# Optimization experiments

Measured on AMD Instinct MI355X. Metric: run time of the kernel, lower is better.

## Reference

```python
import jax, jax.numpy as jnp
import numpy as np

# model dims
B, S, R, D = 2, 64, 2048, 1024      # batch, num_bars(summary len), reg seq len, embed dim
H, KVH, HD = 16, 4, 64              # q heads, kv heads, head dim
G = H // KVH                        # GQA group size
KVD = KVH * HD
TPB = R // S                        # tokens per bar = 32
SCALE = HD ** -0.5
NEG = -1e9


def _rotate_half(x):
    x1, x2 = jnp.split(x, 2, axis=-1)
    return jnp.concatenate([-x2, x1], axis=-1)


def _apply_rope(q, k, cos, sin):
    return q * cos + _rotate_half(q) * sin, k * cos + _rotate_half(k) * sin


def _rope_1d(seq_len):
    # standard RoPE tables, shape (1, 1, seq_len, HD)
    inv = 1.0 / (10000.0 ** (jnp.arange(0, HD, 2, dtype=jnp.float32) / HD))
    freqs = jnp.arange(seq_len, dtype=jnp.float32)[:, None] * inv
    emb = jnp.concatenate([freqs, freqs], axis=-1)
    return jnp.cos(emb)[None, None], jnp.sin(emb)[None, None]


def _rope_2d(bar_ids, tib):
    # hierarchical 2D RoPE: half the rotary freqs encode bar id, half encode token-in-bar id
    q4 = HD // 4
    inv = 1.0 / (10000.0 ** (jnp.arange(q4, dtype=jnp.float32) * 2.0 / (HD // 2)))
    fb = bar_ids.astype(jnp.float32)[..., None] * inv   # (B, R, HD/4)
    ft = tib.astype(jnp.float32)[..., None] * inv       # (B, R, HD/4)
    freqs = jnp.concatenate([fb, ft], axis=-1)          # (B, R, HD/2)
    emb = jnp.concatenate([freqs, freqs], axis=-1)      # (B, R, HD)
    return jnp.cos(emb)[:, None], jnp.sin(emb)[:, None]


def _attn(q, k, v, mask):
    # masked softmax attention; mask (Lq, Lk) broadcast over batch/heads
    s = jnp.einsum('bhqd,bhkd->bhqk', q, k) * SCALE
    s = jnp.where(mask[None, None], s, NEG)
    p = jax.nn.softmax(s, axis=-1)
    return jnp.einsum('bhqk,bhkd->bhqd', p, v)


def _lin(x, w, b):
    return x @ w + b


def _heads(x, n):
    b, l, _ = x.shape
    return x.reshape(b, l, n, HD).transpose(0, 2, 1, 3)


def _merge(x):
    b, h, l, _ = x.shape
    return x.transpose(0, 2, 1, 3).reshape(b, l, h * HD)


PARAM_SHAPES = [('w_sq', (D, D)), ('b_sq', (D,)), ('w_sk', (D, KVD)), ('b_sk', (KVD,)),
                ('w_sv', (D, KVD)), ('b_sv', (KVD,)), ('w_so', (D, D)), ('b_so', (D,)),
                ('w_rq', (D, D)), ('b_rq', (D,)), ('w_rk', (D, KVD)), ('b_rk', (KVD,)),
                ('w_rv', (D, KVD)), ('b_rv', (KVD,)), ('w_ro', (D, D)), ('b_ro', (D,)),
                ('w_k2', (D, KVD)), ('b_k2', (KVD,)), ('w_v2', (D, KVD)), ('b_v2', (KVD,))]


def setup_inputs() -> dict:
    key = jax.random.key(0)
    ks = jax.random.split(key, 2 + len(PARAM_SHAPES))
    inp = {}
    inp['sum_x'] = jax.random.normal(ks[0], (B, S, D), jnp.float32)
    inp['reg_x'] = jax.random.normal(ks[1], (B, R, D), jnp.float32)
    for i, (n, shp) in enumerate(PARAM_SHAPES):
        inp[n] = jax.random.normal(ks[2 + i], shp, jnp.float32) * 0.02
    pos = jnp.arange(R)
    bar = pos // TPB
    tib = pos % TPB
    inp['bar_ids'] = jnp.tile(bar[None], (B, 1)).astype(jnp.int32)
    inp['token_in_bar_ids'] = jnp.tile(tib[None], (B, 1)).astype(jnp.int32)
    # summarize phase: summary-bar i attends to summary j<=i and regular tokens in bars<=i
    key_bar = jnp.concatenate([jnp.arange(S), bar])
    inp['summarize_block_mask'] = key_bar[None, :] <= jnp.arange(S)[:, None]
    # updating phase: regular token t attends to summary-K2 of bars<=bar(t) and regular s<=t
    upd = jnp.concatenate([jnp.arange(S)[None, :] <= bar[:, None],
                           pos[None, :] <= pos[:, None]], axis=1)
    inp['updating_block_mask'] = upd
    return inp


def reference(sum_x, reg_x, w_sq, b_sq, w_sk, b_sk, w_sv, b_sv, w_so, b_so,
              w_rq, b_rq, w_rk, b_rk, w_rv, b_rv, w_ro, b_ro, w_k2, b_k2, w_v2, b_v2,
              summarize_block_mask, updating_block_mask, bar_ids, token_in_bar_ids):
    sum_q = _heads(_lin(sum_x, w_sq, b_sq), H)
    sum_k = _heads(_lin(sum_x, w_sk, b_sk), KVH)
    sum_v = _heads(_lin(sum_x, w_sv, b_sv), KVH)
    reg_q = _heads(_lin(reg_x, w_rq, b_rq), H)
    reg_k = _heads(_lin(reg_x, w_rk, b_rk), KVH)
    reg_v = _heads(_lin(reg_x, w_rv, b_rv), KVH)
    # 1D RoPE for summary tokens, 2D hierarchical RoPE for regular tokens
    cos, sin = _rope_1d(S)
    sum_q, sum_k = _apply_rope(sum_q, sum_k, cos, sin)
    rcos, rsin = _rope_2d(bar_ids, token_in_bar_ids)
    reg_q, reg_k = _apply_rope(reg_q, reg_k, rcos, rsin)
    rep = lambda t: jnp.repeat(t, G, axis=1)  # GQA repeat_interleave over heads
    reg_k_r, reg_v_r = rep(reg_k), rep(reg_v)
    # phase 1: summarize (summary queries over [summary; regular] keys)
    cat_k = jnp.concatenate([rep(sum_k), reg_k_r], axis=2)
    cat_v = jnp.concatenate([rep(sum_v), reg_v_r], axis=2)
    sum_attn = _merge(_attn(sum_q, cat_k, cat_v, summarize_block_mask))  # (B, S, D)
    # phase 2: updating (regular queries over [summary K2/V2; regular] keys)
    k2 = rep(_heads(_lin(sum_attn, w_k2, b_k2), KVH))
    v2 = rep(_heads(_lin(sum_attn, w_v2, b_v2), KVH))
    cat_k2 = jnp.concatenate([k2, reg_k_r], axis=2)
    cat_v2 = jnp.concatenate([v2, reg_v_r], axis=2)
    reg_attn = _merge(_attn(reg_q, cat_k2, cat_v2, updating_block_mask))  # (B, R, D)
    return _lin(sum_attn, w_so, b_so), _lin(reg_attn, w_ro, b_ro)
```

## Files before the change

### kernel.cpp

```cpp
#include <hip/hip_runtime.h>

typedef unsigned short u16;
typedef __attribute__((ext_vector_type(8))) short s8v;
typedef __attribute__((ext_vector_type(4))) float f4v;

#define B_    2
#define S_    64
#define R_    2048
#define D_    1024
#define H_    16
#define KVH_  4
#define LOG2_10K 13.287712379549449f
#define QSC_  0.18033688011112042f

__device__ __forceinline__ u16 f2bf(float f) {
  union { float f; unsigned int i; } v; v.f = f;
  unsigned int x = v.i;
  return (u16)((x + 0x7FFFu + ((x >> 16) & 1u)) >> 16);
}
__device__ __forceinline__ u16 f2bf_ru(float f) {
  union { float f; unsigned int i; } v; v.f = f;
  return (u16)((v.i + 0x8000u) >> 16);
}

__device__ __forceinline__ f4v mfma2(const s8v& a0, const s8v& a1,
                                     const s8v& b0, const s8v& b1) {
  f4v t = {0.f, 0.f, 0.f, 0.f};
  t = __builtin_amdgcn_mfma_f32_16x16x32_bf16(a0, b0, t, 0, 0, 0);
  t = __builtin_amdgcn_mfma_f32_16x16x32_bf16(a1, b1, t, 0, 0, 0);
  return t;
}

struct WT10 { const float* w[10]; u16* o[10]; int C[10]; };

__global__ __launch_bounds__(256)
void transw_k(WT10 ws, const float* __restrict__ xa, const float* __restrict__ xb,
              u16* __restrict__ oa, u16* __restrict__ ob)
{
  const int z = blockIdx.z;
  if (z == 10) {
    int gid = blockIdx.x + blockIdx.y * 32;
    #pragma unroll
    for (int it = 0; it < 3; it++) {
      int idx = gid * 256 + threadIdx.x + it * 262144;
      if (idx < 540672) {
        int i = idx * 8;
        const float* src; u16* dst; int off;
        if (i < 131072) { src = xa; dst = oa; off = i; }
        else            { src = xb; dst = ob; off = i - 131072; }
        float4 a = *(const float4*)(src + off);
        float4 b = *(const float4*)(src + off + 4);
        s8v r;
        r[0] = (short)f2bf(a.x); r[1] = (short)f2bf(a.y);
        r[2] = (short)f2bf(a.z); r[3] = (short)f2bf(a.w);
        r[4] = (short)f2bf(b.x); r[5] = (short)f2bf(b.y);
        r[6] = (short)f2bf(b.z); r[7] = (short)f2bf(b.w);
        *(s8v*)(dst + off) = r;
      }
    }
    return;
  }
  const int C = ws.C[z];
  const int c0 = blockIdx.x * 32, k0 = blockIdx.y * 32;
  if (c0 >= C) return;
  __shared__ float t[32][33];
  const float* w = ws.w[z];
  u16* o = ws.o[z];
  const int x = threadIdx.x & 31, y = threadIdx.x >> 5;
  #pragma unroll
  for (int j = 0; j < 4; j++)
    t[y + 8 * j][x] = w[(size_t)(k0 + y + 8 * j) * C + c0 + x];
  __syncthreads();
  #pragma unroll
  for (int j = 0; j < 4; j++)
    o[(size_t)(c0 + y + 8 * j) * 1024 + k0 + x] = f2bf(t[x][y + 8 * j]);
}

__device__ __forceinline__ void gemm_core_db(
    const u16* __restrict__ Xrow, const u16* __restrict__ WTrow,
    u16 (*Adb)[72], u16 (*Bdb)[72], f4v (&acc)[2][4],
    int tid, int l15, int l4, int wro, int wco)
{
  s8v pa[2], pb[2];
  #pragma unroll
  for (int it = 0; it < 2; it++) {
    int seg = tid + it * 512;
    int r = seg >> 3, sg = (seg & 7) * 8;
    pa[it] = *(const s8v*)(Xrow  + (size_t)r * 1024 + sg);
    pb[it] = *(const s8v*)(WTrow + (size_t)r * 1024 + sg);
  }
  #pragma unroll
  for (int it = 0; it < 2; it++) {
    int seg = tid + it * 512;
    int r = seg >> 3, sg = (seg & 7) * 8;
    *(s8v*)&Adb[r][sg] = pa[it];
    *(s8v*)&Bdb[r][sg] = pb[it];
  }
  __syncthreads();

  #pragma unroll 2
  for (int k = 0; k < 16; k++) {
    const int off = (k & 1) * 128;
    if (k + 1 < 16) {
      const int k0 = (k + 1) * 64;
      #pragma unroll
      for (int it = 0; it < 2; it++) {
        int seg = tid + it * 512;
        int r = seg >> 3, sg = (seg & 7) * 8;
        pa[it] = *(const s8v*)(Xrow  + (size_t)r * 1024 + k0 + sg);
        pb[it] = *(const s8v*)(WTrow + (size_t)r * 1024 + k0 + sg);
      }
    }
    s8v af[2][2], bf4[4][2];
    #pragma unroll
    for (int rc = 0; rc < 2; rc++) {
      af[rc][0] = *(const s8v*)&Adb[off + wro + rc * 16 + l15][l4 * 8];
      af[rc][1] = *(const s8v*)&Adb[off + wro + rc * 16 + l15][32 + l4 * 8];
    }
    #pragma unroll
    for (int cc = 0; cc < 4; cc++) {
      bf4[cc][0] = *(const s8v*)&Bdb[off + wco + cc * 16 + l15][l4 * 8];
      bf4[cc][1] = *(const s8v*)&Bdb[off + wco + cc * 16 + l15][32 + l4 * 8];
    }
    #pragma unroll
    for (int rc = 0; rc < 2; rc++)
      #pragma unroll
      for (int cc = 0; cc < 4; cc++) {
        acc[rc][cc] = __builtin_amdgcn_mfma_f32_16x16x32_bf16(af[rc][0], bf4[cc][0], acc[rc][cc], 0, 0, 0);
        acc[rc][cc] = __builtin_amdgcn_mfma_f32_16x16x32_bf16(af[rc][1], bf4[cc][1], acc[rc][cc], 0, 0, 0);
      }
    if (k + 1 < 16) {
      const int noff = ((k + 1) & 1) * 128;
      #pragma unroll
      for (int it = 0; it < 2; it++) {
        int seg = tid + it * 512;
        int r = seg >> 3, sg = (seg & 7) * 8;
        *(s8v*)&Adb[noff + r][sg] = pa[it];
        *(s8v*)&Bdb[noff + r][sg] = pb[it];
      }
    }
    __syncthreads();
  }
}

__device__ __forceinline__ void epi_to_lds(
    const f4v (&acc)[2][4], const float* __restrict__ Bp, u16* __restrict__ Es,
    int cbr, int wro, int wco, int grb, int LB,
    int ropeMode, bool rope2d, bool sc, int l15, int l4)
{
  float bv[4];
  #pragma unroll
  for (int cc = 0; cc < 4; cc++) bv[cc] = Bp[cbr + cc * 16 + l15];

  if (ropeMode == 0) {
    #pragma unroll
    for (int rc = 0; rc < 2; rc++)
      #pragma unroll
      for (int reg = 0; reg < 4; reg++) {
        int lrow = wro + rc * 16 + l4 * 4 + reg;
        #pragma unroll
        for (int cc = 0; cc < 4; cc++)
          Es[lrow * 136 + wco + cc * 16 + l15] = f2bf(acc[rc][cc][reg] + bv[cc]);
      }
  } else {
    float step = rope2d ? (LOG2_10K / 16.f) : (LOG2_10K / 32.f);
    float inv_lo = exp2f(-(float)l15 * step);
    float inv_hi = rope2d ? inv_lo : inv_lo * exp2f(-16.f * step);
    #pragma unroll
    for (int rc = 0; rc < 2; rc++)
      #pragma unroll
      for (int reg = 0; reg < 4; reg++) {
        int lrow = wro + rc * 16 + l4 * 4 + reg;
        int grow = grb + lrow;
        int pos = grow & (LB - 1);
        int bar = pos >> 5, tib = pos & 31;
        #pragma unroll
        for (int cc = 0; cc < 4; cc++) {
          float inv = (cc & 1) ? inv_hi : inv_lo;
          float bse = rope2d ? (float)((cc & 1) ? tib : bar) : (float)pos;
          float ang = bse * inv;
          float sn, cs;
          sincosf(ang, &sn, &cs);
          float v0 = acc[rc][cc][reg] + bv[cc];
          float v1 = acc[rc][cc ^ 2][reg] + bv[cc ^ 2];
          float rot = (cc < 2) ? -v1 : v1;
          float val = v0 * cs + rot * sn;
          if (sc) val *= QSC_;
          Es[lrow * 136 + wco + cc * 16 + l15] = f2bf(val);
        }
      }
  }
}

__device__ __forceinline__ void store_tile_bf16(
    const u16* __restrict__ Es, u16* __restrict__ out,
    int grb, int c0r, int NH, int LB, int LBS, int tid)
{
  #pragma unroll
  for (int it = 0; it < 4; it++) {
    int idx = it * 512 + tid;
    int r = idx >> 4, ch = idx & 15;
    int grow = grb + r;
    int b = grow >> LBS, pos = grow & (LB - 1);
    int cg = c0r + ch * 8;
    size_t base = (((size_t)b * NH + (cg >> 6)) * LB + pos) * 64 + (cg & 63);
    *(s8v*)(out + base) = *(const s8v*)(Es + r * 136 + ch * 8);
  }
}

__device__ __forceinline__ void store_tile_vT(
    const u16* __restrict__ Es, u16* __restrict__ outT,
    int grb, int kvbase, int LB, int LBS, int tid)
{
  #pragma unroll
  for (int it = 0; it < 4; it++) {
    int idx = tid + it * 512;
    int dcol = idx & 127, rg = idx >> 7;
    int grow = grb + rg * 8;
    int b = grow >> LBS, pos = grow & (LB - 1);
    u16 tmp[8];
    #pragma unroll
    for (int j = 0; j < 8; j++) tmp[j] = Es[(rg * 8 + j) * 136 + dcol];
    u16* dst = outT + (((size_t)(b * KVH_ + kvbase + (dcol >> 6))) * 64 + (dcol & 63)) * LB + pos;
    *(s8v*)dst = *(s8v*)tmp;
  }
}

struct QkvA {
  const u16 *X, *WTs, *WTr;
  const float *b0s, *b1s, *b2s, *b0r, *b1r, *b2r;
  u16 *o0s, *o1s, *o2s, *o0r, *o1r, *o2r;
};

__global__ __launch_bounds__(512)
void qkv_k(QkvA a)
{
  int orig = blockIdx.x;
  int xcd = orig & 7, sidx = orig >> 3;
  int wg = (xcd < 4) ? (xcd * 50 + sidx) : (200 + (xcd - 4) * 49 + sidx);
  const int bx = wg % 12, by = wg / 12;
  const bool issum = (by == 0);
  const int c0 = bx * 128;

  __shared__ u16 Adb[256][72];
  __shared__ u16 Bdb[256][72];
  u16* Es = &Adb[0][0];

  const int tid  = threadIdx.x;
  const int lane = tid & 63;
  const int w    = tid >> 6;
  const int l15  = lane & 15;
  const int l4   = lane >> 4;
  const int wro  = (w >> 1) * 32;
  const int wco  = (w & 1) * 64;

  f4v acc[2][4];
  #pragma unroll
  for (int i = 0; i < 2; i++)
    #pragma unroll
    for (int j = 0; j < 4; j++) acc[i][j] = (f4v){0.f, 0.f, 0.f, 0.f};

  const u16* Xrow  = a.X + (size_t)by * 128 * 1024;
  const u16* WTrow = (issum ? a.WTs : a.WTr) + (size_t)c0 * 1024;
  gemm_core_db(Xrow, WTrow, Adb, Bdb, acc, tid, l15, l4, wro, wco);

  const int LB  = issum ? 64 : 2048;
  const int LBS = issum ? 6 : 11;
  const int grb = issum ? 0 : (by - 1) * 128;

  if (c0 < 1024) {
    epi_to_lds(acc, issum ? a.b0s : a.b0r, Es, c0 + wco, wro, wco, grb, LB, 1, !issum, true, l15, l4);
    __syncthreads();
    store_tile_bf16(Es, issum ? a.o0s : a.o0r, grb, c0, 16, LB, LBS, tid);
  } else if (c0 < 1280) {
    epi_to_lds(acc, issum ? a.b1s : a.b1r, Es, c0 - 1024 + wco, wro, wco, grb, LB, 1, !issum, false, l15, l4);
    __syncthreads();
    store_tile_bf16(Es, issum ? a.o1s : a.o1r, grb, c0 - 1024, 4, LB, LBS, tid);
  } else {
    epi_to_lds(acc, issum ? a.b2s : a.b2r, Es, c0 - 1280 + wco, wro, wco, grb, LB, 0, false, false, l15, l4);
    __syncthreads();
    store_tile_vT(Es, issum ? a.o2s : a.o2r, grb, (c0 - 1280) >> 6, LB, LBS, tid);
  }
}

__global__ __launch_bounds__(512)
void gemm_p1_k(const u16* __restrict__ X, const u16* __restrict__ WT,
               const float* __restrict__ bk2, const float* __restrict__ bv2,
               const float* __restrict__ bso,
               u16* __restrict__ k2, u16* __restrict__ v2T, float* __restrict__ outsum)
{
  const int c0 = blockIdx.x * 128;

  __shared__ u16 Adb[256][72];
  __shared__ u16 Bdb[256][72];
  u16* Es = &Adb[0][0];

  const int tid  = threadIdx.x;
  const int lane = tid & 63;
  const int w    = tid >> 6;
  const int l15  = lane & 15;
  const int l4   = lane >> 4;
  const int wro  = (w >> 1) * 32;
  const int wco  = (w & 1) * 64;

  f4v acc[2][4];
  #pragma unroll
  for (int i = 0; i < 2; i++)
    #pragma unroll
    for (int j = 0; j < 4; j++) acc[i][j] = (f4v){0.f, 0.f, 0.f, 0.f};

  gemm_core_db(X, WT + (size_t)c0 * 1024, Adb, Bdb, acc, tid, l15, l4, wro, wco);

  if (c0 < 256) {
    epi_to_lds(acc, bk2, Es, c0 + wco, wro, wco, 0, 64, 0, false, false, l15, l4);
    __syncthreads();
    store_tile_bf16(Es, k2, 0, c0, 4, 64, 6, tid);
  } else if (c0 < 512) {
    epi_to_lds(acc, bv2, Es, c0 - 256 + wco, wro, wco, 0, 64, 0, false, false, l15, l4);
    __syncthreads();
    store_tile_vT(Es, v2T, 0, (c0 - 256) >> 6, 64, 6, tid);
  } else {
    float bv[4];
    #pragma unroll
    for (int cc = 0; cc < 4; cc++) bv[cc] = bso[c0 - 512 + wco + cc * 16 + l15];
    #pragma unroll
    for (int rc = 0; rc < 2; rc++)
      #pragma unroll
      for (int reg = 0; reg < 4; reg++) {
        int row = wro + rc * 16 + l4 * 4 + reg;
        #pragma unroll
        for (int cc = 0; cc < 4; cc++)
          outsum[(size_t)row * 1024 + c0 - 512 + wco + cc * 16 + l15] = acc[rc][cc][reg] + bv[cc];
      }
  }
}

__global__ __launch_bounds__(512)
void gemm_ro_k(const u16* __restrict__ X, const u16* __restrict__ WT,
               const float* __restrict__ Bp, float* __restrict__ out)
{
  int orig = blockIdx.x;
  int wg = (orig & 7) * 32 + (orig >> 3);
  const int bx = wg & 7, by = wg >> 3;
  const int c0 = bx * 128, r0 = by * 128;

  __shared__ u16 Adb[256][72];
  __shared__ u16 Bdb[256][72];

  const int tid  = threadIdx.x;
  const int lane = tid & 63;
  const int w    = tid >> 6;
  const int l15  = lane & 15;
  const int l4   = lane >> 4;
  const int wro  = (w >> 1) * 32;
  const int wco  = (w & 1) * 64;

  f4v acc[2][4];
  #pragma unroll
  for (int i = 0; i < 2; i++)
    #pragma unroll
    for (int j = 0; j < 4; j++) acc[i][j] = (f4v){0.f, 0.f, 0.f, 0.f};

  gemm_core_db(X + (size_t)r0 * 1024, WT + (size_t)c0 * 1024, Adb, Bdb, acc,
               tid, l15, l4, wro, wco);

  float bv[4];
  #pragma unroll
  for (int cc = 0; cc < 4; cc++) bv[cc] = Bp[c0 + wco + cc * 16 + l15];
  #pragma unroll
  for (int rc = 0; rc < 2; rc++)
    #pragma unroll
    for (int reg = 0; reg < 4; reg++) {
      int row = r0 + wro + rc * 16 + l4 * 4 + reg;
      #pragma unroll
      for (int cc = 0; cc < 4; cc++)
        out[(size_t)row * 1024 + c0 + wco + cc * 16 + l15] = acc[rc][cc][reg] + bv[cc];
    }
}

template<int PHASE>
__device__ __forceinline__ void strip_sm(
    f4v (&s)[4], float& m, float& lsum, f4v (&acc)[4],
    u16 (&PtS)[16][72], bool need_mask, int kbase, int qrow, int l15, int l4)
{
  float tmax = -1e30f;
  if (need_mask) {
    #pragma unroll
    for (int n = 0; n < 4; n++)
      #pragma unroll
      for (int reg = 0; reg < 4; reg++) {
        int kidx = kbase + n * 16 + l4 * 4 + reg;
        bool ok;
        if (kbase == 0) ok = kidx <= ((PHASE == 1) ? qrow : (qrow >> 5));
        else { int kr = kidx - 64; ok = (PHASE == 1) ? ((kr >> 5) <= qrow) : (kr <= qrow); }
        float sv = ok ? s[n][reg] : -1e30f;
        s[n][reg] = sv;
        tmax = fmaxf(tmax, sv);
      }
  } else {
    #pragma unroll
    for (int n = 0; n < 4; n++)
      #pragma unroll
      for (int reg = 0; reg < 4; reg++) tmax = fmaxf(tmax, s[n][reg]);
  }
  tmax = fmaxf(tmax, __shfl_xor(tmax, 16));
  tmax = fmaxf(tmax, __shfl_xor(tmax, 32));

  if (__any(tmax > m)) {
    float mn = fmaxf(m, tmax);
    float f  = __builtin_amdgcn_exp2f(m - mn);
    m = mn;
    lsum *= f;
    #pragma unroll
    for (int dt = 0; dt < 4; dt++)
      #pragma unroll
      for (int reg = 0; reg < 4; reg++) acc[dt][reg] *= f;
  }
  float rsum = 0.f;
  #pragma unroll
  for (int n = 0; n < 4; n++) {
    float p0 = __builtin_amdgcn_exp2f(s[n][0] - m);
    float p1 = __builtin_amdgcn_exp2f(s[n][1] - m);
    float p2 = __builtin_amdgcn_exp2f(s[n][2] - m);
    float p3 = __builtin_amdgcn_exp2f(s[n][3] - m);
    rsum += (p0 + p1) + (p2 + p3);
    uint2 pk;
    pk.x = (unsigned)f2bf_ru(p0) | ((unsigned)f2bf_ru(p1) << 16);
    pk.y = (unsigned)f2bf_ru(p2) | ((unsigned)f2bf_ru(p3) << 16);
    *(uint2*)&PtS[l15][n * 16 + l4 * 4] = pk;
  }
  rsum += __shfl_xor(rsum, 16);
  rsum += __shfl_xor(rsum, 32);
  lsum += rsum;
}

__global__ __launch_bounds__(512)
void attn2_k(const u16* __restrict__ Q, const u16* __restrict__ KS,
             const u16* __restrict__ KR, const u16* __restrict__ VST,
             const u16* __restrict__ VRT, u16* __restrict__ Out)
{
  const int gid = blockIdx.x;
  const int qb  = (gid & 256) ? (15 - (gid & 15)) : (gid & 15);
  const int bh  = gid >> 4;
  const int h   = bh & 15, b = bh >> 4;
  const int q0  = qb * 128;
  const int kh  = h >> 2;

  __shared__ u16 Kt[64][72];
  __shared__ u16 Vt[64][72];
  __shared__ u16 Pt[8][16][72];

  const int tid = threadIdx.x, lane = tid & 63, w = tid >> 6;
  const int l15 = lane & 15, l4 = lane >> 4;
  const int qw  = q0 + w * 16;

  const u16* qp = Q + (((size_t)b * H_ + h) * R_ + qw + l15) * 64;
  s8v qf0 = *(const s8v*)(qp + l4 * 8);
  s8v qf1 = *(const s8v*)(qp + 32 + l4 * 8);

  f4v acc[4];
  #pragma unroll
  for (int dt = 0; dt < 4; dt++) acc[dt] = (f4v){0.f, 0.f, 0.f, 0.f};
  float m = -1e30f, lsum = 0.f;

  const int ntiles = (64 + q0 + 128) >> 6;
  const size_t bh_kv = (size_t)b * KVH_ + kh;
  const int r_ = tid >> 3, sg_ = (tid & 7) * 8;

  {
    const u16* kp = KS  + bh_kv * 4096;
    const u16* vp = VST + bh_kv * 4096;
    s8v k0 = *(const s8v*)(kp + r_ * 64 + sg_);
    s8v v0 = *(const s8v*)(vp + r_ * 64 + sg_);
    *(s8v*)&Kt[r_][sg_] = k0;
    *(s8v*)&Vt[r_][sg_] = v0;
  }
  __syncthreads();

  for (int kt = 0; kt < ntiles; kt++) {
    const int kbase = kt * 64;
    const bool pre = (kt + 1 < ntiles);
    s8v knx, vnx;
    if (pre) {
      const u16* kp = KR  + (bh_kv * R_ + kbase) * 64;
      const u16* vp = VRT + bh_kv * 64 * R_ + kbase;
      knx = *(const s8v*)(kp + r_ * 64 + sg_);
      vnx = *(const s8v*)(vp + (size_t)r_ * R_ + sg_);
    }

    const bool active = (kbase == 0) || (kbase - 64 <= qw + 15);
    if (active) {
      f4v s[4];
      __builtin_amdgcn_s_setprio(1);
      #pragma unroll
      for (int n = 0; n < 4; n++) {
        s8v kf0 = *(const s8v*)&Kt[n * 16 + l15][l4 * 8];
        s8v kf1 = *(const s8v*)&Kt[n * 16 + l15][32 + l4 * 8];
        s[n] = mfma2(kf0, kf1, qf0, qf1);
      }
      __builtin_amdgcn_s_setprio(0);
      bool nm = (kbase == 0) || ((kbase - 1) > qw);
      strip_sm<2>(s, m, lsum, acc, Pt[w], nm, kbase, qw + l15, l15, l4);
      asm volatile("s_waitcnt lgkmcnt(0)" ::: "memory");
      s8v pf0 = *(const s8v*)&Pt[w][l15][l4 * 8];
      s8v pf1 = *(const s8v*)&Pt[w][l15][32 + l4 * 8];
      __builtin_amdgcn_s_setprio(1);
      #pragma unroll
      for (int dt = 0; dt < 4; dt++) {
        s8v vf0 = *(const s8v*)&Vt[dt * 16 + l15][l4 * 8];
        s8v vf1 = *(const s8v*)&Vt[dt * 16 + l15][32 + l4 * 8];
        acc[dt] = __builtin_amdgcn_mfma_f32_16x16x32_bf16(vf0, pf0, acc[dt], 0, 0, 0);
        acc[dt] = __builtin_amdgcn_mfma_f32_16x16x32_bf16(vf1, pf1, acc[dt], 0, 0, 0);
      }
      __builtin_amdgcn_s_setprio(0);
    }

    __syncthreads();
    if (pre) {
      *(s8v*)&Kt[r_][sg_] = knx;
      *(s8v*)&Vt[r_][sg_] = vnx;
      __syncthreads();
    }
  }

  float linv = 1.f / lsum;
  u16* o = Out + ((size_t)b * R_ + qw + l15) * D_ + h * 64;
  #pragma unroll
  for (int dt = 0; dt < 4; dt++) {
    ushort4 t4;
    t4.x = f2bf(acc[dt][0] * linv);
    t4.y = f2bf(acc[dt][1] * linv);
    t4.z = f2bf(acc[dt][2] * linv);
    t4.w = f2bf(acc[dt][3] * linv);
    *(ushort4*)(o + dt * 16 + l4 * 4) = t4;
  }
}

__global__ __launch_bounds__(256)
void attn1_k(const u16* __restrict__ Q, const u16* __restrict__ KS,
             const u16* __restrict__ KR, const u16* __restrict__ VST,
             const u16* __restrict__ VRT,
             float* __restrict__ pO, float* __restrict__ pml)
{
  const int gid = blockIdx.x;
  const int ck  = gid & 7;
  const int bh  = gid >> 3;
  const int h   = bh & 15, b = bh >> 4;
  const int kh  = h >> 2;
  const int kt0 = (ck * 33) >> 3;
  const int kt1 = ((ck + 1) * 33) >> 3;

  __shared__ u16 Kt[2][64][72];
  __shared__ u16 Vt[2][64][72];
  __shared__ u16 Pt[4][16][72];

  const int tid = threadIdx.x, lane = tid & 63, w = tid >> 6;
  const int l15 = lane & 15, l4 = lane >> 4;
  const int qw  = w * 16;

  const u16* qp = Q + (((size_t)b * H_ + h) * S_ + qw + l15) * 64;
  s8v qf0 = *(const s8v*)(qp + l4 * 8);
  s8v qf1 = *(const s8v*)(qp + 32 + l4 * 8);

  f4v acc[4];
  #pragma unroll
  for (int dt = 0; dt < 4; dt++) acc[dt] = (f4v){0.f, 0.f, 0.f, 0.f};
  float m = -1e30f, lsum = 0.f;

  const size_t bh_kv = (size_t)b * KVH_ + kh;
  const int r_ = tid >> 3, sg_ = (tid & 7) * 8;

  {
    const u16 *kp, *vp; int vstr;
    if (kt0 == 0) { kp = KS + bh_kv * 4096; vp = VST + bh_kv * 4096; vstr = 64; }
    else {
      kp = KR  + (bh_kv * R_ + kt0 * 64 - 64) * 64;
      vp = VRT + bh_kv * 64 * R_ + (kt0 * 64 - 64);
      vstr = R_;
    }
    s8v ka0 = *(const s8v*)(kp + r_ * 64 + sg_);
    s8v ka1 = *(const s8v*)(kp + (r_ + 32) * 64 + sg_);
    s8v va0 = *(const s8v*)(vp + (size_t)r_ * vstr + sg_);
    s8v va1 = *(const s8v*)(vp + (size_t)(r_ + 32) * vstr + sg_);
    *(s8v*)&Kt[0][r_][sg_]      = ka0;
    *(s8v*)&Kt[0][r_ + 32][sg_] = ka1;
    *(s8v*)&Vt[0][r_][sg_]      = va0;
    *(s8v*)&Vt[0][r_ + 32][sg_] = va1;
  }
  __syncthreads();

  for (int kt = kt0; kt < kt1; kt++) {
    const int cur = (kt - kt0) & 1;
    const int kbase = kt * 64;
    const bool pre = (kt + 1 < kt1);
    s8v ka0, ka1, va0, va1;
    if (pre) {
      const u16* kp = KR  + (bh_kv * R_ + kbase) * 64;
      const u16* vp = VRT + bh_kv * 64 * R_ + kbase;
      ka0 = *(const s8v*)(kp + r_ * 64 + sg_);
      ka1 = *(const s8v*)(kp + (r_ + 32) * 64 + sg_);
      va0 = *(const s8v*)(vp + (size_t)r_ * R_ + sg_);
      va1 = *(const s8v*)(vp + (size_t)(r_ + 32) * R_ + sg_);
    }

    const bool active = (kbase == 0) || (((kbase - 64) >> 5) <= qw + 15);
    if (active) {
      f4v s[4];
      __builtin_amdgcn_s_setprio(1);
      #pragma unroll
      for (int n = 0; n < 4; n++) {
        s8v kf0 = *(const s8v*)&Kt[cur][n * 16 + l15][l4 * 8];
        s8v kf1 = *(const s8v*)&Kt[cur][n * 16 + l15][32 + l4 * 8];
        s[n] = mfma2(kf0, kf1, qf0, qf1);
      }
      __builtin_amdgcn_s_setprio(0);
      bool nm = (kbase == 0) || (((kbase - 1) >> 5) > qw);
      strip_sm<1>(s, m, lsum, acc, Pt[w], nm, kbase, qw + l15, l15, l4);
      asm volatile("s_waitcnt lgkmcnt(0)" ::: "memory");
      s8v pf0 = *(const s8v*)&Pt[w][l15][l4 * 8];
      s8v pf1 = *(const s8v*)&Pt[w][l15][32 + l4 * 8];
      __builtin_amdgcn_s_setprio(1);
      #pragma unroll
      for (int dt = 0; dt < 4; dt++) {
        s8v vf0 = *(const s8v*)&Vt[cur][dt * 16 + l15][l4 * 8];
        s8v vf1 = *(const s8v*)&Vt[cur][dt * 16 + l15][32 + l4 * 8];
        acc[dt] = __builtin_amdgcn_mfma_f32_16x16x32_bf16(vf0, pf0, acc[dt], 0, 0, 0);
        acc[dt] = __builtin_amdgcn_mfma_f32_16x16x32_bf16(vf1, pf1, acc[dt], 0, 0, 0);
      }
      __builtin_amdgcn_s_setprio(0);
    }

    if (pre) {
      *(s8v*)&Kt[cur ^ 1][r_][sg_]      = ka0;
      *(s8v*)&Kt[cur ^ 1][r_ + 32][sg_] = ka1;
      *(s8v*)&Vt[cur ^ 1][r_][sg_]      = va0;
      *(s8v*)&Vt[cur ^ 1][r_ + 32][sg_] = va1;
    }
    __syncthreads();
  }

  float* po = pO + (((size_t)ck * 32 + bh) * 64 + qw + l15) * 64;
  #pragma unroll
  for (int dt = 0; dt < 4; dt++)
    *(f4v*)(po + dt * 16 + l4 * 4) = acc[dt];
  if (l4 == 0) {
    float* pm = pml + (((size_t)ck * 32 + bh) * 64 + qw + l15) * 2;
    pm[0] = m; pm[1] = lsum;
  }
}

__global__ __launch_bounds__(256)
void comb1_k(const float* __restrict__ pO, const float* __restrict__ pml,
             u16* __restrict__ sattn)
{
  const int bh = blockIdx.x;
  const int b = bh >> 4, h = bh & 15;
  const int q  = threadIdx.x >> 2;
  const int d0 = (threadIdx.x & 3) * 16;
  float mv[8], lv[8], mstar = -1e30f;
  #pragma unroll
  for (int c = 0; c < 8; c++) {
    const float* p = pml + (((size_t)c * 32 + bh) * 64 + q) * 2;
    mv[c] = p[0]; lv[c] = p[1];
    mstar = fmaxf(mstar, mv[c]);
  }
  float o[16];
  #pragma unroll
  for (int j = 0; j < 16; j++) o[j] = 0.f;
  float lsum = 0.f;
  #pragma unroll
  for (int c = 0; c < 8; c++) {
    float wgt = __builtin_amdgcn_exp2f(mv[c] - mstar);
    lsum += lv[c] * wgt;
    const float* po = pO + (((size_t)c * 32 + bh) * 64 + q) * 64 + d0;
    #pragma unroll
    for (int j = 0; j < 16; j++) o[j] += po[j] * wgt;
  }
  float inv = 1.f / lsum;
  u16 ob[16];
  #pragma unroll
  for (int j = 0; j < 16; j++) ob[j] = f2bf(o[j] * inv);
  u16* out = sattn + ((size_t)(b * 64 + q)) * 1024 + h * 64 + d0;
  *(s8v*)out       = *(s8v*)&ob[0];
  *(s8v*)(out + 8) = *(s8v*)&ob[8];
}

extern "C" void kernel_launch(void* const* d_in, const int* in_sizes, int n_in,
                              void* d_out, int out_size, void* d_ws, size_t ws_size,
                              hipStream_t stream)
{
  (void)out_size; (void)ws_size;

  static const int expect[22] = {
    131072, 4194304,
    1048576, 1024, 262144, 256,
    262144, 256, 1048576, 1024,
    1048576, 1024, 262144, 256,
    262144, 256, 1048576, 1024,
    262144, 256, 262144, 256
  };
  if (n_in < 22) return;
  for (int i = 0; i < 22; i++) if (in_sizes[i] != expect[i]) return;

  const float* sum_x = (const float*)d_in[0];
  const float* reg_x = (const float*)d_in[1];
  const float* w_sq = (const float*)d_in[2];  const float* b_sq = (const float*)d_in[3];
  const float* w_sk = (const float*)d_in[4];  const float* b_sk = (const float*)d_in[5];
  const float* w_sv = (const float*)d_in[6];  const float* b_sv = (const float*)d_in[7];
  const float* w_so = (const float*)d_in[8];  const float* b_so = (const float*)d_in[9];
  const float* w_rq = (const float*)d_in[10]; const float* b_rq = (const float*)d_in[11];
  const float* w_rk = (const float*)d_in[12]; const float* b_rk = (const float*)d_in[13];
  const float* w_rv = (const float*)d_in[14]; const float* b_rv = (const float*)d_in[15];
  const float* w_ro = (const float*)d_in[16]; const float* b_ro = (const float*)d_in[17];
  const float* w_k2 = (const float*)d_in[18]; const float* b_k2 = (const float*)d_in[19];
  const float* w_v2 = (const float*)d_in[20]; const float* b_v2 = (const float*)d_in[21];

  u16* ws    = (u16*)d_ws;
  u16* xs_bf = ws;
  u16* xr_bf = xs_bf + 131072;
  u16* wt_s  = xr_bf + 4194304;
  u16* wt_r  = wt_s  + 1572864;
  u16* wt_p  = wt_r  + 1572864;
  u16* wt_ro = wt_p  + 1572864;
  u16* sq    = wt_ro + 1048576;
  u16* sk    = sq    + 131072;
  u16* svT   = sk    + 32768;
  u16* rq    = svT   + 32768;
  u16* rk    = rq    + 4194304;
  u16* rvT   = rk    + 1048576;
  u16* sattn = rvT   + 1048576;
  u16* k2    = sattn + 131072;
  u16* v2T   = k2    + 32768;
  u16* rattn = v2T   + 32768;

  float* pO  = (float*)rattn;
  float* pml = pO + 1048576;

  float* out_sum = (float*)d_out;
  float* out_reg = out_sum + 131072;

  dim3 blk(256);

  WT10 wt;
  wt.w[0] = w_sq; wt.o[0] = wt_s;              wt.C[0] = 1024;
  wt.w[1] = w_rq; wt.o[1] = wt_r;              wt.C[1] = 1024;
  wt.w[2] = w_so; wt.o[2] = wt_p + 512 * 1024; wt.C[2] = 1024;
  wt.w[3] = w_ro; wt.o[3] = wt_ro;             wt.C[3] = 1024;
  wt.w[4] = w_sk; wt.o[4] = wt_s + 1024 * 1024; wt.C[4] = 256;
  wt.w[5] = w_sv; wt.o[5] = wt_s + 1280 * 1024; wt.C[5] = 256;
  wt.w[6] = w_rk; wt.o[6] = wt_r + 1024 * 1024; wt.C[6] = 256;
  wt.w[7] = w_rv; wt.o[7] = wt_r + 1280 * 1024; wt.C[7] = 256;
  wt.w[8] = w_k2; wt.o[8] = wt_p;               wt.C[8] = 256;
  wt.w[9] = w_v2; wt.o[9] = wt_p + 256 * 1024;  wt.C[9] = 256;
  transw_k<<<dim3(32, 32, 11), blk, 0, stream>>>(wt, sum_x, reg_x, xs_bf, xr_bf);

  QkvA qa;
  qa.X = xs_bf; qa.WTs = wt_s; qa.WTr = wt_r;
  qa.b0s = b_sq; qa.b1s = b_sk; qa.b2s = b_sv;
  qa.b0r = b_rq; qa.b1r = b_rk; qa.b2r = b_rv;
  qa.o0s = sq; qa.o1s = sk; qa.o2s = svT;
  qa.o0r = rq; qa.o1r = rk; qa.o2r = rvT;
  qkv_k<<<dim3(396), dim3(512), 0, stream>>>(qa);

  attn1_k<<<dim3(256), blk, 0, stream>>>(sq, sk, rk, svT, rvT, pO, pml);
  comb1_k<<<dim3(32), blk, 0, stream>>>(pO, pml, sattn);

  gemm_p1_k<<<dim3(12), dim3(512), 0, stream>>>(sattn, wt_p, b_k2, b_v2, b_so, k2, v2T, out_sum);

  attn2_k<<<dim3(512), dim3(512), 0, stream>>>(rq, k2, rk, v2T, rvT, rattn);

  gemm_ro_k<<<dim3(256), dim3(512), 0, stream>>>(rattn, wt_ro, b_ro, out_reg);
}
```

Before: 134.8 us.

## Load GEMM tiles directly to LDS with XOR-swizzled layout, single buffer

Replaces the register-staged, double-buffered GEMM mainloop with global_load_lds direct-to-LDS copies into a single 128x64 tile per operand, using an XOR swizzle instead of row padding to avoid bank conflicts. This removes VGPR staging and LDS write instructions and cuts LDS footprint, which may raise occupancy. The trade-off is losing the overlap of next-tile global loads with MFMA work, since each iteration now waits on two barriers around the load.

```diff
diff --git a/kernel.cpp b/kernel.cpp
--- a/kernel.cpp
+++ b/kernel.cpp
@@ -76,51 +76,48 @@
     o[(size_t)(c0 + y + 8 * j) * 1024 + k0 + x] = f2bf(t[x][y + 8 * j]);
 }
 
-__device__ __forceinline__ void gemm_core_db(
+__device__ __forceinline__ void gemm_core_gl(
     const u16* __restrict__ Xrow, const u16* __restrict__ WTrow,
-    u16 (*Adb)[72], u16 (*Bdb)[72], f4v (&acc)[2][4],
+    u16* __restrict__ As, u16* __restrict__ Bs, f4v (&acc)[2][4],
     int tid, int l15, int l4, int wro, int wco)
 {
-  s8v pa[2], pb[2];
-  #pragma unroll
-  for (int it = 0; it < 2; it++) {
-    int seg = tid + it * 512;
-    int r = seg >> 3, sg = (seg & 7) * 8;
-    pa[it] = *(const s8v*)(Xrow  + (size_t)r * 1024 + sg);
-    pb[it] = *(const s8v*)(WTrow + (size_t)r * 1024 + sg);
-  }
-  #pragma unroll
-  for (int it = 0; it < 2; it++) {
-    int seg = tid + it * 512;
-    int r = seg >> 3, sg = (seg & 7) * 8;
-    *(s8v*)&Adb[r][sg] = pa[it];
-    *(s8v*)&Bdb[r][sg] = pb[it];
-  }
-  __syncthreads();
-
-  #pragma unroll 2
+  const int w    = tid >> 6;
+  const int lane = tid & 63;
+  const int rl   = lane >> 3;
+  const int c8   = lane & 7;
+  const int x7   = l15 & 7;
+  const int csw  = (c8 ^ rl) * 8;
+
   for (int k = 0; k < 16; k++) {
-    const int off = (k & 1) * 128;
-    if (k + 1 < 16) {
-      const int k0 = (k + 1) * 64;
-      #pragma unroll
-      for (int it = 0; it < 2; it++) {
-        int seg = tid + it * 512;
-        int r = seg >> 3, sg = (seg & 7) * 8;
-        pa[it] = *(const s8v*)(Xrow  + (size_t)r * 1024 + k0 + sg);
-        pb[it] = *(const s8v*)(WTrow + (size_t)r * 1024 + k0 + sg);
-      }
-    }
+    const int k0 = k * 64;
+    __syncthreads();
+    #pragma unroll
+    for (int j = 0; j < 2; j++) {
+      int rbase = w * 16 + j * 8;
+      int r = rbase + rl;
+      __builtin_amdgcn_global_load_lds(
+        (const __attribute__((address_space(1))) void*)(Xrow + (size_t)r * 1024 + k0 + csw),
+        (__attribute__((address_space(3))) void*)(As + rbase * 64),
+        16, 0, 0);
+      __builtin_amdgcn_global_load_lds(
+        (const __attribute__((address_space(1))) void*)(WTrow + (size_t)r * 1024 + k0 + csw),
+        (__attribute__((address_space(3))) void*)(Bs + rbase * 64),
+        16, 0, 0);
+    }
+    __syncthreads();
+
     s8v af[2][2], bf4[4][2];
     #pragma unroll
     for (int rc = 0; rc < 2; rc++) {
-      af[rc][0] = *(const s8v*)&Adb[off + wro + rc * 16 + l15][l4 * 8];
-      af[rc][1] = *(const s8v*)&Adb[off + wro + rc * 16 + l15][32 + l4 * 8];
+      int row = wro + rc * 16 + l15;
+      af[rc][0] = *(const s8v*)(As + row * 64 + ((l4 ^ x7) * 8));
+      af[rc][1] = *(const s8v*)(As + row * 64 + (((l4 + 4) ^ x7) * 8));
     }
     #pragma unroll
     for (int cc = 0; cc < 4; cc++) {
-      bf4[cc][0] = *(const s8v*)&Bdb[off + wco + cc * 16 + l15][l4 * 8];
-      bf4[cc][1] = *(const s8v*)&Bdb[off + wco + cc * 16 + l15][32 + l4 * 8];
+      int row = wco + cc * 16 + l15;
+      bf4[cc][0] = *(const s8v*)(Bs + row * 64 + ((l4 ^ x7) * 8));
+      bf4[cc][1] = *(const s8v*)(Bs + row * 64 + (((l4 + 4) ^ x7) * 8));
     }
     #pragma unroll
     for (int rc = 0; rc < 2; rc++)
@@ -129,18 +126,8 @@
         acc[rc][cc] = __builtin_amdgcn_mfma_f32_16x16x32_bf16(af[rc][0], bf4[cc][0], acc[rc][cc], 0, 0, 0);
         acc[rc][cc] = __builtin_amdgcn_mfma_f32_16x16x32_bf16(af[rc][1], bf4[cc][1], acc[rc][cc], 0, 0, 0);
       }
-    if (k + 1 < 16) {
-      const int noff = ((k + 1) & 1) * 128;
-      #pragma unroll
-      for (int it = 0; it < 2; it++) {
-        int seg = tid + it * 512;
-        int r = seg >> 3, sg = (seg & 7) * 8;
-        *(s8v*)&Adb[noff + r][sg] = pa[it];
-        *(s8v*)&Bdb[noff + r][sg] = pb[it];
-      }
-    }
-    __syncthreads();
-  }
+  }
+  __syncthreads();
 }
 
 __device__ __forceinline__ void epi_to_lds(
@@ -242,9 +229,10 @@
   const bool issum = (by == 0);
   const int c0 = bx * 128;
 
-  __shared__ u16 Adb[256][72];
-  __shared__ u16 Bdb[256][72];
-  u16* Es = &Adb[0][0];
+  __shared__ u16 LDSU[17408];
+  u16* As = LDSU;
+  u16* Bs = LDSU + 8192;
+  u16* Es = LDSU;
 
   const int tid  = threadIdx.x;
   const int lane = tid & 63;
@@ -262,7 +250,7 @@
 
   const u16* Xrow  = a.X + (size_t)by * 128 * 1024;
   const u16* WTrow = (issum ? a.WTs : a.WTr) + (size_t)c0 * 1024;
-  gemm_core_db(Xrow, WTrow, Adb, Bdb, acc, tid, l15, l4, wro, wco);
+  gemm_core_gl(Xrow, WTrow, As, Bs, acc, tid, l15, l4, wro, wco);
 
   const int LB  = issum ? 64 : 2048;
   const int LBS = issum ? 6 : 11;
@@ -291,9 +279,10 @@
 {
   const int c0 = blockIdx.x * 128;
 
-  __shared__ u16 Adb[256][72];
-  __shared__ u16 Bdb[256][72];
-  u16* Es = &Adb[0][0];
+  __shared__ u16 LDSU[17408];
+  u16* As = LDSU;
+  u16* Bs = LDSU + 8192;
+  u16* Es = LDSU;
 
   const int tid  = threadIdx.x;
   const int lane = tid & 63;
@@ -309,7 +298,7 @@
     #pragma unroll
     for (int j = 0; j < 4; j++) acc[i][j] = (f4v){0.f, 0.f, 0.f, 0.f};
 
-  gemm_core_db(X, WT + (size_t)c0 * 1024, Adb, Bdb, acc, tid, l15, l4, wro, wco);
+  gemm_core_gl(X, WT + (size_t)c0 * 1024, As, Bs, acc, tid, l15, l4, wro, wco);
 
   if (c0 < 256) {
     epi_to_lds(acc, bk2, Es, c0 + wco, wro, wco, 0, 64, 0, false, false, l15, l4);
@@ -344,8 +333,9 @@
   const int bx = wg & 7, by = wg >> 3;
   const int c0 = bx * 128, r0 = by * 128;
 
-  __shared__ u16 Adb[256][72];
-  __shared__ u16 Bdb[256][72];
+  __shared__ u16 LDSU[16384];
+  u16* As = LDSU;
+  u16* Bs = LDSU + 8192;
 
   const int tid  = threadIdx.x;
   const int lane = tid & 63;
@@ -361,7 +351,7 @@
     #pragma unroll
     for (int j = 0; j < 4; j++) acc[i][j] = (f4v){0.f, 0.f, 0.f, 0.f};
 
-  gemm_core_db(X + (size_t)r0 * 1024, WT + (size_t)c0 * 1024, Adb, Bdb, acc,
+  gemm_core_gl(X + (size_t)r0 * 1024, WT + (size_t)c0 * 1024, As, Bs, acc,
                tid, l15, l4, wro, wco);
 
   float bv[4];
```

Measured after the change: 132.5 us. Within noise of the previous version (-1.6%).
